# Performance work log

Hardware: AMD Instinct MI355X
Metric: run time of the kernel (lower is better)

## Reference

```python
import jax, jax.numpy as jnp
import numpy as np

D2, D1, T1, T2, D3, T3 = 120, 40, 10, 5, 3, 1


def _kaiming_uniform(key, shape):
    # torch kaiming_uniform_ with nonlinearity='relu': bound = sqrt(6/fan_in), fan_in = shape[1]
    bound = np.sqrt(6.0 / shape[1])
    return jax.random.uniform(key, shape, jnp.float32, -bound, bound)


def setup_inputs() -> dict:
    key = jax.random.key(0)
    ks = jax.random.split(key, 6)
    x = jax.random.normal(ks[0], (131072, D1, T1), jnp.float32)
    return {
        "x": x,
        "BL_W1": _kaiming_uniform(ks[1], (D2, D1)),
        "BL_W2": _kaiming_uniform(ks[2], (T1, T2)),
        "BL_B": jnp.zeros((D2, T2), jnp.float32),
        "T_W1": _kaiming_uniform(ks[3], (D3, D2)),
        "T_W": jnp.full((T2, T2), 1.0 / T2, jnp.float32),
        "T_W2": _kaiming_uniform(ks[4], (T2, T3)),
        "T_B": jnp.zeros((D3, T3), jnp.float32),
        "l": jnp.full((1,), 0.5, jnp.float32),
    }


def _max_norm(w):
    # torch max_norm_: if frobenius norm > 10, rescale to norm 10 (done under no_grad)
    n = jnp.linalg.norm(w)
    scale = jnp.where(n > 10.0, 10.0 / (1e-8 + n), 1.0)
    return w * jax.lax.stop_gradient(scale)


def reference(x, BL_W1, BL_W2, BL_B, T_W1, T_W, T_W2, T_B, l):
    # --- weight clamps performed at the top of m_btabl.forward ---
    W1a = _max_norm(BL_W1)
    W2a = _max_norm(BL_W2)
    W1b = _max_norm(T_W1)
    Wb = _max_norm(T_W)
    W2b = _max_norm(T_W2)
    lam = jnp.clip(l[0], 0.0, 1.0)  # l.data clamped to [0,1]

    # BL layer: relu(W1 @ x @ W2 + B); x: [B, D1, T1] -> [B, D2, T2]
    h = jax.nn.relu(jnp.einsum('ed,bdt->bet', W1a, x) @ W2a + BL_B)
    # dropout(0.1) is identity at inference

    # TABL layer (t1 here = T2 = 5)
    X = jnp.einsum('ed,bdt->bet', W1b, h)          # [B, D3, T2]
    eye = jnp.eye(T2, dtype=jnp.float32)
    Wm = Wb - Wb * eye + eye / T2                  # force diagonal to 1/t1
    A = jax.nn.softmax(X @ Wm, axis=-1)            # temporal attention
    X = lam * X + (1.0 - lam) * X * A              # convex combination
    y = X @ W2b + T_B                              # [B, D3, 1]

    y = jnp.squeeze(y)                             # [B, D3]
    return jax.nn.softmax(y, axis=1)
```

## Files before the change

### kernel.cpp

```cpp
#include <hip/hip_runtime.h>


typedef short bf16x8 __attribute__((ext_vector_type(8)));
typedef float f32x4v __attribute__((ext_vector_type(4)));

#define NTP 256
#define NTM 320

__device__ __forceinline__ unsigned short f2bf(float f) {
    unsigned int u = __float_as_uint(f);
    u += 0x7FFFu + ((u >> 16) & 1u);
    return (unsigned short)(u >> 16);
}

__device__ __forceinline__ float block_reduce_sum(float v, float* red, int tid) {
    #pragma unroll
    for (int off = 32; off > 0; off >>= 1) v += __shfl_xor(v, off, 64);
    if ((tid & 63) == 0) red[tid >> 6] = v;
    __syncthreads();
    float r = red[0] + red[1] + red[2] + red[3];
    __syncthreads();
    return r;
}

__global__ __launch_bounds__(NTP)
void prep_kernel(const float* __restrict__ W1, const float* __restrict__ W2,
                 const float* __restrict__ B,  const float* __restrict__ Tw1,
                 const float* __restrict__ Tw, const float* __restrict__ Tw2,
                 const float* __restrict__ TB, const float* __restrict__ l,
                 float* __restrict__ ws)
{
    __shared__ float red[4];
    const int tid = threadIdx.x;
    float ss;
    ss = 0.f; for (int i = tid; i < 4800; i += NTP) { float w = W1[i];  ss += w*w; }
    const float n1 = sqrtf(block_reduce_sum(ss, red, tid));
    ss = 0.f; for (int i = tid; i < 50;   i += NTP) { float w = W2[i];  ss += w*w; }
    const float n2 = sqrtf(block_reduce_sum(ss, red, tid));
    ss = 0.f; for (int i = tid; i < 360;  i += NTP) { float w = Tw1[i]; ss += w*w; }
    const float n3 = sqrtf(block_reduce_sum(ss, red, tid));
    ss = 0.f; for (int i = tid; i < 25;   i += NTP) { float w = Tw[i];  ss += w*w; }
    const float n4 = sqrtf(block_reduce_sum(ss, red, tid));
    ss = 0.f; for (int i = tid; i < 5;    i += NTP) { float w = Tw2[i]; ss += w*w; }
    const float n5 = sqrtf(block_reduce_sum(ss, red, tid));

    const float s1 = n1 > 10.f ? 10.f/(1e-8f+n1) : 1.f;
    const float s2 = n2 > 10.f ? 10.f/(1e-8f+n2) : 1.f;
    const float s3 = n3 > 10.f ? 10.f/(1e-8f+n3) : 1.f;
    const float s4 = n4 > 10.f ? 10.f/(1e-8f+n4) : 1.f;
    const float s5 = n5 > 10.f ? 10.f/(1e-8f+n5) : 1.f;

    unsigned short* img = (unsigned short*)ws;
    for (int i = tid; i < 129*48; i += NTP) {
        const int e = i / 48, k = i - e*48;
        float v = 0.f;
        if (e < 120) {
            if (k < 40)      v = W1[e*40 + k] * s1;
            else if (k < 45) v = B[e*5 + (k-40)];
        }
        img[i] = f2bf(v);
    }
    for (int i = tid; i < 512; i += NTP) {
        const int e = i >> 2, c = i & 3;
        ws[3096 + i] = (c < 3 && e < 120) ? Tw1[c*120 + e] * s3 : 0.f;
    }
    for (int i = tid; i < 36; i += NTP) {
        float v = 0.f;
        if (i < 25)      { int r = i/5, c = i - r*5; v = (r == c) ? 0.2f : Tw[i]*s4; }
        else if (i < 30) v = Tw2[i-25] * s5;
        else if (i < 33) v = TB[i-30];
        else if (i == 33){ float lv = l[0]; v = fminf(fmaxf(lv, 0.f), 1.f); }
        ws[3608 + i] = v;
    }
    for (int i = tid; i < 50; i += NTP) ws[3644 + i] = W2[i] * s2;
}

__global__ __launch_bounds__(NTM)
void btabl_main(const float* __restrict__ x, const float* __restrict__ ws,
                float* __restrict__ out, int nsamp)
{
    __align__(16) __shared__ unsigned short sW1[129*48];
    __align__(16) __shared__ float          sWp[128*4];
    __align__(16) __shared__ float          sC[36];
    __align__(16) __shared__ unsigned short sZ[320*48 + 16];
    __align__(16) __shared__ float          sX3[320*3];

    const int tid = threadIdx.x;

    {
        const float4* src = (const float4*)ws;
        float4* d1 = (float4*)sW1;
        for (int i = tid; i < 774; i += NTM) d1[i] = src[i];
        float4* d2 = (float4*)sWp;
        for (int i = tid; i < 128; i += NTM) d2[i] = src[774 + i];
        if (tid < 9) ((float4*)sC)[tid] = src[902 + tid];
    }

    {
        const int sLoc = tid / 5, c = tid - sLoc*5;
        const int sGlob = blockIdx.x * 64 + sLoc;
        const int sClamp = sGlob < nsamp ? sGlob : (nsamp - 1);
        const float* W2p = ws + 3644;
        const float* xs = x + (size_t)sClamp*400 + c*80;

        float Zf[8][5];
        #pragma unroll
        for (int hh = 0; hh < 2; hh++) {
            const float4* xv = (const float4*)(xs + hh*40);
            float xf[40];
            #pragma unroll
            for (int i = 0; i < 10; i++) {
                float4 q = xv[i];
                xf[i*4+0] = q.x; xf[i*4+1] = q.y; xf[i*4+2] = q.z; xf[i*4+3] = q.w;
            }
            #pragma unroll
            for (int r = 0; r < 4; r++) {
                #pragma unroll
                for (int t = 0; t < 5; t++) {
                    float a = 0.f;
                    #pragma unroll
                    for (int k = 0; k < 10; k++)
                        a = fmaf(xf[r*10+k], W2p[k*5+t], a);
                    Zf[hh*4+r][t] = a;
                }
            }
        }
        const int colBase = 5 * sLoc;
        #pragma unroll
        for (int t = 0; t < 5; t++) {
            bf16x8 zv;
            #pragma unroll
            for (int r = 0; r < 8; r++) zv[r] = (short)f2bf(Zf[r][t]);
            *(bf16x8*)(sZ + (colBase + t)*48 + c*8) = zv;
        }
        bf16x8 oh = {0,0,0,0,0,0,0,0};
        oh[c] = (short)0x3F80;
        *(bf16x8*)(sZ + (colBase + c)*48 + 40) = oh;
    }
    __syncthreads();

    const int wave = tid >> 6;
    const int lane = tid & 63;
    const int quad = lane >> 4;
    const int m    = lane & 15;
    const int colBase = wave * 64;

    bf16x8 Bf[4][2];
    const bf16x8 z8 = {0,0,0,0,0,0,0,0};
    #pragma unroll
    for (int nt = 0; nt < 4; nt++) {
        const int col = colBase + nt*16 + m;
        Bf[nt][0] = *(const bf16x8*)(sZ + col*48 + quad*8);
        bf16x8 b1 = *(const bf16x8*)(sZ + col*48 + 32 + quad*8);
        Bf[nt][1] = (quad >= 2) ? z8 : b1;
    }

    float X3p[4][3];
    #pragma unroll
    for (int nt = 0; nt < 4; nt++)
        #pragma unroll
        for (int j = 0; j < 3; j++) X3p[nt][j] = 0.f;

    const f32x4v zacc = {0.f, 0.f, 0.f, 0.f};
    #pragma unroll
    for (int mt = 0; mt < 8; mt++) {
        const unsigned short* arow = sW1 + (mt*16 + m)*48;
        const bf16x8 A0 = *(const bf16x8*)(arow + quad*8);
        const bf16x8 A1 = *(const bf16x8*)(arow + 32 + quad*8);
        f32x4v wp[4];
        #pragma unroll
        for (int r = 0; r < 4; r++)
            wp[r] = *(const f32x4v*)(sWp + (mt*16 + quad*4 + r)*4);
        #pragma unroll
        for (int nt = 0; nt < 4; nt++) {
            f32x4v acc = __builtin_amdgcn_mfma_f32_16x16x32_bf16(A0, Bf[nt][0], zacc, 0, 0, 0);
            acc = __builtin_amdgcn_mfma_f32_16x16x32_bf16(A1, Bf[nt][1], acc, 0, 0, 0);
            #pragma unroll
            for (int r = 0; r < 4; r++) {
                const float h = fmaxf(acc[r], 0.f);
                X3p[nt][0] = fmaf(wp[r][0], h, X3p[nt][0]);
                X3p[nt][1] = fmaf(wp[r][1], h, X3p[nt][1]);
                X3p[nt][2] = fmaf(wp[r][2], h, X3p[nt][2]);
            }
        }
    }

    #pragma unroll
    for (int nt = 0; nt < 4; nt++) {
        #pragma unroll
        for (int j = 0; j < 3; j++) {
            float v = X3p[nt][j];
            v += __shfl_xor(v, 16, 64);
            v += __shfl_xor(v, 32, 64);
            X3p[nt][j] = v;
        }
    }
    if (quad == 0) {
        #pragma unroll
        for (int nt = 0; nt < 4; nt++) {
            const int col = colBase + nt*16 + m;
            sX3[col*3 + 0] = X3p[nt][0];
            sX3[col*3 + 1] = X3p[nt][1];
            sX3[col*3 + 2] = X3p[nt][2];
        }
    }
    __syncthreads();

    if (tid < 64) {
        const int sGlob = blockIdx.x * 64 + tid;
        float X3v[3][5];
        #pragma unroll
        for (int t = 0; t < 5; t++)
            #pragma unroll
            for (int j = 0; j < 3; j++)
                X3v[j][t] = sX3[(tid*5 + t)*3 + j];

        const float lam  = sC[33];
        const float olam = 1.f - lam;
        float y[3];
        #pragma unroll
        for (int j = 0; j < 3; j++) {
            float S[5];
            #pragma unroll
            for (int t = 0; t < 5; t++) {
                float a = 0.f;
                #pragma unroll
                for (int k = 0; k < 5; k++)
                    a = fmaf(X3v[j][k], sC[k*5 + t], a);
                S[t] = a;
            }
            float mx = S[0];
            #pragma unroll
            for (int t = 1; t < 5; t++) mx = fmaxf(mx, S[t]);
            float ex[5], se = 0.f;
            #pragma unroll
            for (int t = 0; t < 5; t++) { ex[t] = __expf(S[t] - mx); se += ex[t]; }
            const float inv = 1.f / se;
            float yj = sC[30 + j];
            #pragma unroll
            for (int t = 0; t < 5; t++) {
                const float a  = ex[t] * inv;
                const float xc = X3v[j][t] * (lam + olam * a);
                yj = fmaf(xc, sC[25 + t], yj);
            }
            y[j] = yj;
        }
        const float mx = fmaxf(y[0], fmaxf(y[1], y[2]));
        const float e0 = __expf(y[0]-mx), e1 = __expf(y[1]-mx), e2 = __expf(y[2]-mx);
        const float inv = 1.f / (e0 + e1 + e2);
        if (sGlob < nsamp) {
            float* o = out + (size_t)sGlob*3;
            o[0] = e0*inv; o[1] = e1*inv; o[2] = e2*inv;
        }
    }
}

extern "C" void kernel_launch(void* const* d_in, const int* in_sizes, int n_in,
                              void* d_out, int out_size, void* d_ws, size_t ws_size,
                              hipStream_t stream) {
    const float* x   = (const float*)d_in[0];
    const float* W1  = (const float*)d_in[1];
    const float* W2  = (const float*)d_in[2];
    const float* B   = (const float*)d_in[3];
    const float* Tw1 = (const float*)d_in[4];
    const float* Tw  = (const float*)d_in[5];
    const float* Tw2 = (const float*)d_in[6];
    const float* TB  = (const float*)d_in[7];
    const float* l   = (const float*)d_in[8];
    float* out = (float*)d_out;
    float* ws  = (float*)d_ws;

    hipLaunchKernelGGL(prep_kernel, dim3(1), dim3(NTP), 0, stream,
                       W1, W2, B, Tw1, Tw, Tw2, TB, l, ws);

    const int nsamp = in_sizes[0] / 400;
    const int grid  = (nsamp + 63) / 64;
    hipLaunchKernelGGL(btabl_main, dim3(grid), dim3(NTM), 0, stream,
                       x, ws, out, nsamp);
}
```

Before: 380.6 us.

## Fuse weight prep into persistent main kernel with per-wave sample groups

Removes the separate single-block prep kernel and builds the normalized weight images directly in each block's shared memory. The main kernel becomes a persistent grid of 768 blocks where each wave independently loops over 16-sample groups with private LDS staging, eliminating block-wide barriers in the hot loop. The cost is redundant weight-norm reduction in every block and more work per wave; the data mapping for the first contraction is also reorganized.

```diff
diff --git a/kernel.cpp b/kernel.cpp
--- a/kernel.cpp
+++ b/kernel.cpp
@@ -4,8 +4,9 @@
 typedef short bf16x8 __attribute__((ext_vector_type(8)));
 typedef float f32x4v __attribute__((ext_vector_type(4)));
 
-#define NTP 256
-#define NTM 320
+#define NT   256
+#define WPB  4
+#define GRID 768
 
 __device__ __forceinline__ unsigned short f2bf(float f) {
     unsigned int u = __float_as_uint(f);
@@ -23,25 +24,34 @@
     return r;
 }
 
-__global__ __launch_bounds__(NTP)
-void prep_kernel(const float* __restrict__ W1, const float* __restrict__ W2,
-                 const float* __restrict__ B,  const float* __restrict__ Tw1,
-                 const float* __restrict__ Tw, const float* __restrict__ Tw2,
-                 const float* __restrict__ TB, const float* __restrict__ l,
-                 float* __restrict__ ws)
+__global__ __launch_bounds__(NT)
+void btabl_fused(const float* __restrict__ x,  const float* __restrict__ W1,
+                 const float* __restrict__ W2, const float* __restrict__ B,
+                 const float* __restrict__ Tw1,const float* __restrict__ Tw,
+                 const float* __restrict__ Tw2,const float* __restrict__ TB,
+                 const float* __restrict__ l,  float* __restrict__ out,
+                 int nsamp)
 {
+    __align__(16) __shared__ unsigned short sW1[128*48 + 16];
+    __align__(16) __shared__ float          sWp[128*4];
+    __align__(16) __shared__ float          sW2[52];
+    __align__(16) __shared__ float          sC[36];
+    __align__(16) __shared__ unsigned short sZ[WPB][80*48+16];
+    __align__(16) __shared__ float          sX3[WPB][80*3];
     __shared__ float red[4];
+
     const int tid = threadIdx.x;
+
     float ss;
-    ss = 0.f; for (int i = tid; i < 4800; i += NTP) { float w = W1[i];  ss += w*w; }
+    ss = 0.f; for (int i = tid; i < 4800; i += NT) { float w = W1[i];  ss += w*w; }
     const float n1 = sqrtf(block_reduce_sum(ss, red, tid));
-    ss = 0.f; for (int i = tid; i < 50;   i += NTP) { float w = W2[i];  ss += w*w; }
+    ss = 0.f; for (int i = tid; i < 50;   i += NT) { float w = W2[i];  ss += w*w; }
     const float n2 = sqrtf(block_reduce_sum(ss, red, tid));
-    ss = 0.f; for (int i = tid; i < 360;  i += NTP) { float w = Tw1[i]; ss += w*w; }
+    ss = 0.f; for (int i = tid; i < 360;  i += NT) { float w = Tw1[i]; ss += w*w; }
     const float n3 = sqrtf(block_reduce_sum(ss, red, tid));
-    ss = 0.f; for (int i = tid; i < 25;   i += NTP) { float w = Tw[i];  ss += w*w; }
+    ss = 0.f; for (int i = tid; i < 25;   i += NT) { float w = Tw[i];  ss += w*w; }
     const float n4 = sqrtf(block_reduce_sum(ss, red, tid));
-    ss = 0.f; for (int i = tid; i < 5;    i += NTP) { float w = Tw2[i]; ss += w*w; }
+    ss = 0.f; for (int i = tid; i < 5;    i += NT) { float w = Tw2[i]; ss += w*w; }
     const float n5 = sqrtf(block_reduce_sum(ss, red, tid));
 
     const float s1 = n1 > 10.f ? 10.f/(1e-8f+n1) : 1.f;
@@ -50,207 +60,184 @@
     const float s4 = n4 > 10.f ? 10.f/(1e-8f+n4) : 1.f;
     const float s5 = n5 > 10.f ? 10.f/(1e-8f+n5) : 1.f;
 
-    unsigned short* img = (unsigned short*)ws;
-    for (int i = tid; i < 129*48; i += NTP) {
+    for (int i = tid; i < 128*48+16; i += NT) {
         const int e = i / 48, k = i - e*48;
         float v = 0.f;
         if (e < 120) {
             if (k < 40)      v = W1[e*40 + k] * s1;
             else if (k < 45) v = B[e*5 + (k-40)];
         }
-        img[i] = f2bf(v);
-    }
-    for (int i = tid; i < 512; i += NTP) {
+        sW1[i] = f2bf(v);
+    }
+    for (int i = tid; i < 512; i += NT) {
         const int e = i >> 2, c = i & 3;
-        ws[3096 + i] = (c < 3 && e < 120) ? Tw1[c*120 + e] * s3 : 0.f;
-    }
-    for (int i = tid; i < 36; i += NTP) {
+        sWp[i] = (c < 3 && e < 120) ? Tw1[c*120 + e] * s3 : 0.f;
+    }
+    for (int i = tid; i < 52; i += NT) sW2[i] = (i < 50) ? W2[i]*s2 : 0.f;
+    for (int i = tid; i < 36; i += NT) {
         float v = 0.f;
         if (i < 25)      { int r = i/5, c = i - r*5; v = (r == c) ? 0.2f : Tw[i]*s4; }
         else if (i < 30) v = Tw2[i-25] * s5;
         else if (i < 33) v = TB[i-30];
         else if (i == 33){ float lv = l[0]; v = fminf(fmaxf(lv, 0.f), 1.f); }
-        ws[3608 + i] = v;
-    }
-    for (int i = tid; i < 50; i += NTP) ws[3644 + i] = W2[i] * s2;
-}
-
-__global__ __launch_bounds__(NTM)
-void btabl_main(const float* __restrict__ x, const float* __restrict__ ws,
-                float* __restrict__ out, int nsamp)
-{
-    __align__(16) __shared__ unsigned short sW1[129*48];
-    __align__(16) __shared__ float          sWp[128*4];
-    __align__(16) __shared__ float          sC[36];
-    __align__(16) __shared__ unsigned short sZ[320*48 + 16];
-    __align__(16) __shared__ float          sX3[320*3];
-
-    const int tid = threadIdx.x;
+        sC[i] = v;
+    }
+    __syncthreads();
+
+    const int wv   = tid >> 6;
+    const int lane = tid & 63;
+    const int quad = lane >> 4;
+    const int m    = lane & 15;
+    const int sLoc = lane >> 2;
+    const int cc   = lane & 3;
+
+    unsigned short* zp  = &sZ[wv][0];
+    float*          x3p = &sX3[wv][0];
 
     {
-        const float4* src = (const float4*)ws;
-        float4* d1 = (float4*)sW1;
-        for (int i = tid; i < 774; i += NTM) d1[i] = src[i];
-        float4* d2 = (float4*)sWp;
-        for (int i = tid; i < 128; i += NTM) d2[i] = src[774 + i];
-        if (tid < 9) ((float4*)sC)[tid] = src[902 + tid];
-    }
-
-    {
-        const int sLoc = tid / 5, c = tid - sLoc*5;
-        const int sGlob = blockIdx.x * 64 + sLoc;
-        const int sClamp = sGlob < nsamp ? sGlob : (nsamp - 1);
-        const float* W2p = ws + 3644;
-        const float* xs = x + (size_t)sClamp*400 + c*80;
-
-        float Zf[8][5];
-        #pragma unroll
-        for (int hh = 0; hh < 2; hh++) {
-            const float4* xv = (const float4*)(xs + hh*40);
-            float xf[40];
-            #pragma unroll
-            for (int i = 0; i < 10; i++) {
-                float4 q = xv[i];
-                xf[i*4+0] = q.x; xf[i*4+1] = q.y; xf[i*4+2] = q.z; xf[i*4+3] = q.w;
-            }
-            #pragma unroll
-            for (int r = 0; r < 4; r++) {
+        unsigned int* z32 = (unsigned int*)zp;
+        for (int col = lane; col < 80; col += 64) {
+            const int t = col % 5;
+            const int base = col*24 + 20;
+            #pragma unroll
+            for (int j = 0; j < 4; j++) z32[base + j] = 0u;
+            z32[base + (t >> 1)] = (t & 1) ? 0x3F800000u : 0x00003F80u;
+        }
+    }
+
+    const int ngroups = (nsamp + 15) >> 4;
+    const int wid     = blockIdx.x * WPB + wv;
+    const float lam   = sC[33];
+    const float olam  = 1.f - lam;
+
+    for (int g = wid; g < ngroups; g += GRID*WPB) {
+        {
+            const int sG  = g*16 + sLoc;
+            const int sCl = sG < nsamp ? sG : nsamp - 1;
+            const float* xs = x + (size_t)sCl*400 + cc*100;
+
+            float w2l[50];
+            #pragma unroll
+            for (int i = 0; i < 50; i++) w2l[i] = sW2[i];
+
+            const int colB = sLoc * 5;
+            #pragma unroll
+            for (int pr = 0; pr < 5; pr++) {
+                const float4* xv = (const float4*)(xs + pr*20);
+                float4 a0 = xv[0], a1 = xv[1], a2 = xv[2], a3 = xv[3], a4 = xv[4];
+                const float v[20] = {a0.x,a0.y,a0.z,a0.w, a1.x,a1.y,a1.z,a1.w,
+                                     a2.x,a2.y,a2.z,a2.w, a3.x,a3.y,a3.z,a3.w,
+                                     a4.x,a4.y,a4.z,a4.w};
+                #pragma unroll
+                for (int t = 0; t < 5; t++) {
+                    float z0 = 0.f, z1 = 0.f;
+                    #pragma unroll
+                    for (int k = 0; k < 10; k++) {
+                        z0 = fmaf(v[k],      w2l[k*5+t], z0);
+                        z1 = fmaf(v[10+k],   w2l[k*5+t], z1);
+                    }
+                    const unsigned int dw =
+                        (unsigned int)f2bf(z0) | ((unsigned int)f2bf(z1) << 16);
+                    *(unsigned int*)(zp + (colB + t)*48 + cc*10 + pr*2) = dw;
+                }
+            }
+        }
+
+        bf16x8 Bf0[5], Bf1[5];
+        const bf16x8 z8 = {0,0,0,0,0,0,0,0};
+        #pragma unroll
+        for (int nt = 0; nt < 5; nt++) {
+            const unsigned short* bcol = zp + (nt*16 + m)*48;
+            Bf0[nt] = *(const bf16x8*)(bcol + quad*8);
+            bf16x8 b1 = *(const bf16x8*)(bcol + 32 + quad*8);
+            Bf1[nt] = (quad >= 2) ? z8 : b1;
+        }
+
+        float X3p[5][3];
+        #pragma unroll
+        for (int nt = 0; nt < 5; nt++)
+            #pragma unroll
+            for (int j = 0; j < 3; j++) X3p[nt][j] = 0.f;
+
+        const f32x4v zac = {0.f,0.f,0.f,0.f};
+        #pragma unroll
+        for (int mt = 0; mt < 8; mt++) {
+            const unsigned short* ar = sW1 + (mt*16 + m)*48;
+            const bf16x8 A0 = *(const bf16x8*)(ar + quad*8);
+            const bf16x8 A1 = *(const bf16x8*)(ar + 32 + quad*8);
+            f32x4v wp[4];
+            #pragma unroll
+            for (int r = 0; r < 4; r++)
+                wp[r] = *(const f32x4v*)(sWp + (mt*16 + quad*4 + r)*4);
+            #pragma unroll
+            for (int nt = 0; nt < 5; nt++) {
+                f32x4v acc = __builtin_amdgcn_mfma_f32_16x16x32_bf16(A0, Bf0[nt], zac, 0,0,0);
+                acc = __builtin_amdgcn_mfma_f32_16x16x32_bf16(A1, Bf1[nt], acc, 0,0,0);
+                #pragma unroll
+                for (int r = 0; r < 4; r++) {
+                    const float h = fmaxf(acc[r], 0.f);
+                    X3p[nt][0] = fmaf(wp[r][0], h, X3p[nt][0]);
+                    X3p[nt][1] = fmaf(wp[r][1], h, X3p[nt][1]);
+                    X3p[nt][2] = fmaf(wp[r][2], h, X3p[nt][2]);
+                }
+            }
+        }
+
+        #pragma unroll
+        for (int nt = 0; nt < 5; nt++) {
+            #pragma unroll
+            for (int j = 0; j < 3; j++) {
+                float v = X3p[nt][j];
+                v += __shfl_xor(v, 16, 64);
+                v += __shfl_xor(v, 32, 64);
+                if (quad == 0) x3p[(nt*16 + m)*3 + j] = v;
+            }
+        }
+
+        if (lane < 16) {
+            float X3v[3][5];
+            #pragma unroll
+            for (int t = 0; t < 5; t++)
+                #pragma unroll
+                for (int j = 0; j < 3; j++)
+                    X3v[j][t] = x3p[(lane*5 + t)*3 + j];
+
+            float y[3];
+            #pragma unroll
+            for (int j = 0; j < 3; j++) {
+                float S[5];
                 #pragma unroll
                 for (int t = 0; t < 5; t++) {
                     float a = 0.f;
                     #pragma unroll
-                    for (int k = 0; k < 10; k++)
-                        a = fmaf(xf[r*10+k], W2p[k*5+t], a);
-                    Zf[hh*4+r][t] = a;
-                }
-            }
-        }
-        const int colBase = 5 * sLoc;
-        #pragma unroll
-        for (int t = 0; t < 5; t++) {
-            bf16x8 zv;
-            #pragma unroll
-            for (int r = 0; r < 8; r++) zv[r] = (short)f2bf(Zf[r][t]);
-            *(bf16x8*)(sZ + (colBase + t)*48 + c*8) = zv;
-        }
-        bf16x8 oh = {0,0,0,0,0,0,0,0};
-        oh[c] = (short)0x3F80;
-        *(bf16x8*)(sZ + (colBase + c)*48 + 40) = oh;
-    }
-    __syncthreads();
-
-    const int wave = tid >> 6;
-    const int lane = tid & 63;
-    const int quad = lane >> 4;
-    const int m    = lane & 15;
-    const int colBase = wave * 64;
-
-    bf16x8 Bf[4][2];
-    const bf16x8 z8 = {0,0,0,0,0,0,0,0};
-    #pragma unroll
-    for (int nt = 0; nt < 4; nt++) {
-        const int col = colBase + nt*16 + m;
-        Bf[nt][0] = *(const bf16x8*)(sZ + col*48 + quad*8);
-        bf16x8 b1 = *(const bf16x8*)(sZ + col*48 + 32 + quad*8);
-        Bf[nt][1] = (quad >= 2) ? z8 : b1;
-    }
-
-    float X3p[4][3];
-    #pragma unroll
-    for (int nt = 0; nt < 4; nt++)
-        #pragma unroll
-        for (int j = 0; j < 3; j++) X3p[nt][j] = 0.f;
-
-    const f32x4v zacc = {0.f, 0.f, 0.f, 0.f};
-    #pragma unroll
-    for (int mt = 0; mt < 8; mt++) {
-        const unsigned short* arow = sW1 + (mt*16 + m)*48;
-        const bf16x8 A0 = *(const bf16x8*)(arow + quad*8);
-        const bf16x8 A1 = *(const bf16x8*)(arow + 32 + quad*8);
-        f32x4v wp[4];
-        #pragma unroll
-        for (int r = 0; r < 4; r++)
-            wp[r] = *(const f32x4v*)(sWp + (mt*16 + quad*4 + r)*4);
-        #pragma unroll
-        for (int nt = 0; nt < 4; nt++) {
-            f32x4v acc = __builtin_amdgcn_mfma_f32_16x16x32_bf16(A0, Bf[nt][0], zacc, 0, 0, 0);
-            acc = __builtin_amdgcn_mfma_f32_16x16x32_bf16(A1, Bf[nt][1], acc, 0, 0, 0);
-            #pragma unroll
-            for (int r = 0; r < 4; r++) {
-                const float h = fmaxf(acc[r], 0.f);
-                X3p[nt][0] = fmaf(wp[r][0], h, X3p[nt][0]);
-                X3p[nt][1] = fmaf(wp[r][1], h, X3p[nt][1]);
-                X3p[nt][2] = fmaf(wp[r][2], h, X3p[nt][2]);
-            }
-        }
-    }
-
-    #pragma unroll
-    for (int nt = 0; nt < 4; nt++) {
-        #pragma unroll
-        for (int j = 0; j < 3; j++) {
-            float v = X3p[nt][j];
-            v += __shfl_xor(v, 16, 64);
-            v += __shfl_xor(v, 32, 64);
-            X3p[nt][j] = v;
-        }
-    }
-    if (quad == 0) {
-        #pragma unroll
-        for (int nt = 0; nt < 4; nt++) {
-            const int col = colBase + nt*16 + m;
-            sX3[col*3 + 0] = X3p[nt][0];
-            sX3[col*3 + 1] = X3p[nt][1];
-            sX3[col*3 + 2] = X3p[nt][2];
-        }
-    }
-    __syncthreads();
-
-    if (tid < 64) {
-        const int sGlob = blockIdx.x * 64 + tid;
-        float X3v[3][5];
-        #pragma unroll
-        for (int t = 0; t < 5; t++)
-            #pragma unroll
-            for (int j = 0; j < 3; j++)
-                X3v[j][t] = sX3[(tid*5 + t)*3 + j];
-
-        const float lam  = sC[33];
-        const float olam = 1.f - lam;
-        float y[3];
-        #pragma unroll
-        for (int j = 0; j < 3; j++) {
-            float S[5];
-            #pragma unroll
-            for (int t = 0; t < 5; t++) {
-                float a = 0.f;
-                #pragma unroll
-                for (int k = 0; k < 5; k++)
-                    a = fmaf(X3v[j][k], sC[k*5 + t], a);
-                S[t] = a;
-            }
-            float mx = S[0];
-            #pragma unroll
-            for (int t = 1; t < 5; t++) mx = fmaxf(mx, S[t]);
-            float ex[5], se = 0.f;
-            #pragma unroll
-            for (int t = 0; t < 5; t++) { ex[t] = __expf(S[t] - mx); se += ex[t]; }
-            const float inv = 1.f / se;
-            float yj = sC[30 + j];
-            #pragma unroll
-            for (int t = 0; t < 5; t++) {
-                const float a  = ex[t] * inv;
-                const float xc = X3v[j][t] * (lam + olam * a);
-                yj = fmaf(xc, sC[25 + t], yj);
-            }
-            y[j] = yj;
-        }
-        const float mx = fmaxf(y[0], fmaxf(y[1], y[2]));
-        const float e0 = __expf(y[0]-mx), e1 = __expf(y[1]-mx), e2 = __expf(y[2]-mx);
-        const float inv = 1.f / (e0 + e1 + e2);
-        if (sGlob < nsamp) {
-            float* o = out + (size_t)sGlob*3;
-            o[0] = e0*inv; o[1] = e1*inv; o[2] = e2*inv;
+                    for (int k = 0; k < 5; k++)
+                        a = fmaf(X3v[j][k], sC[k*5 + t], a);
+                    S[t] = a;
+                }
+                float mx = S[0];
+                #pragma unroll
+                for (int t = 1; t < 5; t++) mx = fmaxf(mx, S[t]);
+                float ex[5], se = 0.f;
+                #pragma unroll
+                for (int t = 0; t < 5; t++) { ex[t] = __expf(S[t]-mx); se += ex[t]; }
+                const float inv = 1.f / se;
+                float yj = sC[30 + j];
+                #pragma unroll
+                for (int t = 0; t < 5; t++) {
+                    const float a  = ex[t] * inv;
+                    const float xc = X3v[j][t] * (lam + olam * a);
+                    yj = fmaf(xc, sC[25 + t], yj);
+                }
+                y[j] = yj;
+            }
+            const float mx = fmaxf(y[0], fmaxf(y[1], y[2]));
+            const float e0 = __expf(y[0]-mx), e1 = __expf(y[1]-mx), e2 = __expf(y[2]-mx);
+            const float inv = 1.f / (e0 + e1 + e2);
+            const int sG = g*16 + lane;
+            if (sG < nsamp) {
+                float* o = out + (size_t)sG*3;
+                o[0] = e0*inv; o[1] = e1*inv; o[2] = e2*inv;
+            }
         }
     }
 }
@@ -268,13 +255,8 @@
     const float* TB  = (const float*)d_in[7];
     const float* l   = (const float*)d_in[8];
     float* out = (float*)d_out;
-    float* ws  = (float*)d_ws;
-
-    hipLaunchKernelGGL(prep_kernel, dim3(1), dim3(NTP), 0, stream,
-                       W1, W2, B, Tw1, Tw, Tw2, TB, l, ws);
 
     const int nsamp = in_sizes[0] / 400;
-    const int grid  = (nsamp + 63) / 64;
-    hipLaunchKernelGGL(btabl_main, dim3(grid), dim3(NTM), 0, stream,
-                       x, ws, out, nsamp);
-}
+    hipLaunchKernelGGL(btabl_fused, dim3(GRID), dim3(NT), 0, stream,
+                       x, W1, W2, B, Tw1, Tw, Tw2, TB, l, out, nsamp);
+}
```

Result: slower. 457.0 us (+20.1%).
